# Performance work log

Hardware: AMD Instinct MI355X
Metric: run time of the kernel (lower is better)

The kernel has to match this reference:

```python
import jax, jax.numpy as jnp
import numpy as np

N = 100000      # nodes
E = 1600000     # edges (avg degree 16)
FEAT, HID, OUT = 128, 64, 40
P_DROP = 0.5


def setup_inputs() -> dict:
    key = jax.random.key(0)
    ks = jax.random.split(key, 7)
    x = jax.random.normal(ks[0], (N, FEAT), dtype=jnp.float32)
    edge_index = jax.random.randint(ks[1], (2, E), 0, N, dtype=jnp.int32)
    W1 = jax.random.normal(ks[2], (FEAT, HID), dtype=jnp.float32) / np.float32(np.sqrt(FEAT))
    b1 = jnp.zeros((HID,), jnp.float32)
    W2 = jax.random.normal(ks[3], (HID, OUT), dtype=jnp.float32) / np.float32(np.sqrt(HID))
    b2 = jnp.zeros((OUT,), jnp.float32)
    # scaled inverted-dropout mask: values in {0, 1/(1-p)}
    keep = jax.random.bernoulli(ks[4], 1.0 - P_DROP, (N, HID))
    drop_mask = keep.astype(jnp.float32) / np.float32(1.0 - P_DROP)
    return {"x": x, "edge_index": edge_index, "W1": W1, "b1": b1,
            "W2": W2, "b2": b2, "drop_mask": drop_mask}


def _gcn_conv(x, W, b, src, dst):
    """PyG GCNConv: h = xW; add self-loops; sym-normalized scatter-add; +b."""
    h = x @ W                                   # [N, D_out]
    ones = jnp.ones((src.shape[0],), h.dtype)
    deg = jax.ops.segment_sum(ones, dst, num_segments=N) + 1.0  # +1 self-loop
    dinv = jax.lax.rsqrt(deg)                   # deg > 0 due to self-loops
    norm = dinv[src] * dinv[dst]                # [E]
    msg = h[src] * norm[:, None]                # gather + scale
    agg = jax.ops.segment_sum(msg, dst, num_segments=N)
    agg = agg + h * (dinv * dinv)[:, None]      # self-loop contribution
    return agg + b


def reference(x, edge_index, W1, b1, W2, b2, drop_mask):
    src, dst = edge_index[0], edge_index[1]
    h = _gcn_conv(x, W1, b1, src, dst)
    h = jax.nn.relu(h)
    h = h * drop_mask                           # F.dropout (pre-drawn mask)
    out = _gcn_conv(h, W2, b2, src, dst)
    return out
```

## Files before the change

kernel.cpp:

```cpp
#include <hip/hip_runtime.h>
#include <hip/hip_fp16.h>

#define NN     100000
#define NE     1600000
#define FEAT   128
#define HID    64
#define OUTD   40
#define BNODES 32
#define NSB    ((NN + 255) / 256)
#define NBAGG  (NSB * 8)
#define CAP    5120
#define CCHUNK 2048
#define WSCALE 262144.0f
#define WINV   (1.0f / 262144.0f)

typedef _Float16 half8 __attribute__((ext_vector_type(8)));
typedef float    f32x4 __attribute__((ext_vector_type(4)));

__global__ __launch_bounds__(256) void k_pairs(const int* __restrict__ src,
                                               const int* __restrict__ dst,
                                               int* __restrict__ bfill,
                                               int* __restrict__ pairs) {
    __shared__ int bcnt[NSB];
    __shared__ int gb[NSB];
    int t = threadIdx.x;
    for (int i = t; i < NSB; i += 256) bcnt[i] = 0;
    __syncthreads();
    int e0 = blockIdx.x * CCHUNK;
    int pk[8], bb[8], off[8];
    #pragma unroll
    for (int i = 0; i < 8; ++i) {
        int e = e0 + i * 256 + t;
        if (e < NE) {
            int d = dst[e];
            pk[i]  = (src[e] << 8) | (d & 255);
            bb[i]  = d >> 8;
            off[i] = atomicAdd(&bcnt[bb[i]], 1);
        } else bb[i] = -1;
    }
    __syncthreads();
    for (int i = t; i < NSB; i += 256) {
        int c = bcnt[i];
        gb[i] = c ? (i * CAP + atomicAdd(&bfill[i], c)) : 0;
    }
    __syncthreads();
    #pragma unroll
    for (int i = 0; i < 8; ++i)
        if (bb[i] >= 0) pairs[gb[bb[i]] + off[i]] = pk[i];
}

__global__ __launch_bounds__(256) void k_degdinv(const int* __restrict__ pairs,
                                                 const int* __restrict__ bfill,
                                                 float* __restrict__ dinv) {
    __shared__ int hist[256];
    int b = blockIdx.x, t = threadIdx.x;
    hist[t] = 0;
    __syncthreads();
    int base = b * CAP, count = bfill[b];
    for (int i = t; i < count; i += 256)
        atomicAdd(&hist[pairs[base + i] & 255], 1);
    __syncthreads();
    int node = (b << 8) + t;
    if (node < NN) dinv[node] = rsqrtf((float)hist[t] + 1.0f);
}

__global__ __launch_bounds__(256) void k_csr(const int* __restrict__ pairs,
                                             const int* __restrict__ bfill,
                                             int* __restrict__ sb_beg,
                                             int* __restrict__ sb_cnt,
                                             int* __restrict__ csr) {
    __shared__ int hist[2048];
    __shared__ int exs[2048];
    __shared__ int part[256];
    __shared__ int poff[9];
    __shared__ int sstart[8];
    __shared__ int dtot[8];
    int b = blockIdx.x, t = threadIdx.x;
    #pragma unroll
    for (int k = 0; k < 8; ++k) hist[t * 8 + k] = 0;
    __syncthreads();
    int base = b * CAP, count = bfill[b];
    for (int i = t; i < count; i += 256) {
        int p = pairs[base + i];
        int key = (((p & 255) >> 5) << 8) | ((p >> 17) & 255);
        atomicAdd(&hist[key], 1);
    }
    __syncthreads();
    int loc[8], s0 = 0;
    #pragma unroll
    for (int k = 0; k < 8; ++k) { loc[k] = s0; s0 += hist[t * 8 + k]; }
    part[t] = s0;
    __syncthreads();
    for (int off = 1; off < 256; off <<= 1) {
        int u = (t >= off) ? part[t - off] : 0;
        __syncthreads();
        part[t] += u;
        __syncthreads();
    }
    int pex = part[t] - s0;
    #pragma unroll
    for (int k = 0; k < 8; ++k) exs[t * 8 + k] = pex + loc[k];
    __syncthreads();
    if (t < 8) {
        sstart[t] = exs[t * 256];
        int end = (t == 7) ? count : exs[(t + 1) * 256];
        dtot[t] = end - sstart[t];
    }
    __syncthreads();
    if (t == 0) {
        poff[0] = 0;
        for (int d = 0; d < 8; ++d) poff[d + 1] = poff[d] + ((dtot[d] + 31) & ~31);
    }
    __syncthreads();
    #pragma unroll
    for (int k = 0; k < 8; ++k) {
        int key = t * 8 + k;
        int d = key >> 8;
        exs[key] = poff[d] + (exs[key] - sstart[d]);
        hist[key] = 0;
    }
    __syncthreads();
    for (int i = t; i < count; i += 256) {
        int p = pairs[base + i];
        int key = (((p & 255) >> 5) << 8) | ((p >> 17) & 255);
        int pos = exs[key] + atomicAdd(&hist[key], 1);
        csr[base + pos] = ((p >> 8) << 7) | (p & 31);
    }
    for (int d = 0; d < 8; ++d) {
        int padded = (dtot[d] + 31) & ~31;
        for (int i = dtot[d] + t; i < padded; i += 256)
            csr[base + poff[d] + i] = (NN << 7);
    }
    if (t < 8) {
        sb_beg[b * 8 + t] = base + poff[t];
        sb_cnt[b * 8 + t] = (dtot[t] + 31) & ~31;
    }
}

__global__ __launch_bounds__(256) void k_maskbits(const float* __restrict__ mask,
                                                  unsigned long long* __restrict__ mb) {
    int node = blockIdx.x * 4 + (threadIdx.x >> 6);
    if (node >= NN) return;
    int l = threadIdx.x & 63;
    float m = mask[(size_t)node * HID + l];
    unsigned long long bits = __ballot(m != 0.f);
    if (l == 0) mb[node] = bits;
}

__global__ __launch_bounds__(256) void k_wprep(const float* __restrict__ W1,
                                               const float* __restrict__ W2,
                                               _Float16* __restrict__ w1f,
                                               _Float16* __restrict__ w2f,
                                               __half* __restrict__ h1s,
                                               __half* __restrict__ hhs) {
    int t = threadIdx.x;
    for (int it = t; it < 16 * 64; it += 256) {
        int f = it >> 6, l = it & 63;
        int kk = f >> 2, n = f & 3;
        int krow = kk * 32 + (l >> 4) * 8;
        int col  = n * 16 + (l & 15);
        #pragma unroll
        for (int i = 0; i < 8; ++i)
            w1f[it * 8 + i] = (_Float16)W1[(krow + i) * HID + col];
    }
    for (int it = t; it < 6 * 64; it += 256) {
        int f = it >> 6, l = it & 63;
        int kk = f / 3, n = f - kk * 3;
        int krow = kk * 32 + (l >> 4) * 8;
        int col  = n * 16 + (l & 15);
        #pragma unroll
        for (int i = 0; i < 8; ++i)
            w2f[it * 8 + i] = (col < OUTD) ? (_Float16)W2[(krow + i) * OUTD + col]
                                           : (_Float16)0.f;
    }
    if (t < HID) {
        h1s[(size_t)NN * HID + t] = __float2half(0.f);
        hhs[(size_t)NN * HID + t] = __float2half(0.f);
    }
}

__global__ __launch_bounds__(256) void k_mgemm1(const float* __restrict__ x,
                                                const _Float16* __restrict__ w1f,
                                                const float* __restrict__ dinv,
                                                __half* __restrict__ h1s) {
    int wid = (blockIdx.x * 256 + threadIdx.x) >> 6;
    int l = threadIdx.x & 63;
    if (wid >= NN / 16) return;
    half8 bf[4][4];
    #pragma unroll
    for (int kk = 0; kk < 4; ++kk)
        #pragma unroll
        for (int n = 0; n < 4; ++n)
            bf[kk][n] = ((const half8*)w1f)[(kk * 4 + n) * 64 + l];
    f32x4 acc[4] = {};
    int arow = wid * 16 + (l & 15);
    const float* xp = x + (size_t)arow * FEAT + (l >> 4) * 8;
    #pragma unroll
    for (int kk = 0; kk < 4; ++kk) {
        float4 u0 = *(const float4*)(xp + kk * 32);
        float4 u1 = *(const float4*)(xp + kk * 32 + 4);
        half8 af;
        af[0] = (_Float16)u0.x; af[1] = (_Float16)u0.y;
        af[2] = (_Float16)u0.z; af[3] = (_Float16)u0.w;
        af[4] = (_Float16)u1.x; af[5] = (_Float16)u1.y;
        af[6] = (_Float16)u1.z; af[7] = (_Float16)u1.w;
        #pragma unroll
        for (int n = 0; n < 4; ++n)
            acc[n] = __builtin_amdgcn_mfma_f32_16x16x32_f16(af, bf[kk][n], acc[n], 0, 0, 0);
    }
    int orow = wid * 16 + (l >> 4) * 4;
    int ocol = l & 15;
    float dv[4];
    #pragma unroll
    for (int r = 0; r < 4; ++r) dv[r] = dinv[orow + r];
    #pragma unroll
    for (int n = 0; n < 4; ++n)
        #pragma unroll
        for (int r = 0; r < 4; ++r)
            h1s[(size_t)(orow + r) * HID + n * 16 + ocol] = __float2half(acc[n][r] * dv[r]);
}

template<int MODE>
__global__ __launch_bounds__(256) void k_bagg(const int* __restrict__ csr,
                                              const int* __restrict__ sb_beg,
                                              const int* __restrict__ sb_cnt,
                                              const float* __restrict__ dinv,
                                              const __half* __restrict__ feat,
                                              const float* __restrict__ b1,
                                              const unsigned long long* __restrict__ maskbits,
                                              __half* __restrict__ outp) {
    __shared__ int acc[BNODES * HID];
    int t = threadIdx.x, wv = t >> 6, l = t & 63;
    int bb = blockIdx.x;
    int4* a4 = (int4*)acc;
    for (int i = t; i < BNODES * HID / 4; i += 256) a4[i] = make_int4(0, 0, 0, 0);
    __syncthreads();
    int base  = sb_beg[bb];
    int count = sb_cnt[bb];
    int node0 = (bb >> 3) * 256 + (bb & 7) * 32;
    const char* fb = (const char*)feat + ((size_t)l * 2);
    for (int j = wv * 8; j < count; j += 32) {
        int e0 = csr[base + j + 0], e1 = csr[base + j + 1];
        int e2 = csr[base + j + 2], e3 = csr[base + j + 3];
        int e4 = csr[base + j + 4], e5 = csr[base + j + 5];
        int e6 = csr[base + j + 6], e7 = csr[base + j + 7];
        float a0 = __half2float(*(const __half*)(fb + (unsigned)(e0 & ~127)));
        float a1 = __half2float(*(const __half*)(fb + (unsigned)(e1 & ~127)));
        float a2 = __half2float(*(const __half*)(fb + (unsigned)(e2 & ~127)));
        float a3 = __half2float(*(const __half*)(fb + (unsigned)(e3 & ~127)));
        float a4v = __half2float(*(const __half*)(fb + (unsigned)(e4 & ~127)));
        float a5 = __half2float(*(const __half*)(fb + (unsigned)(e5 & ~127)));
        float a6 = __half2float(*(const __half*)(fb + (unsigned)(e6 & ~127)));
        float a7 = __half2float(*(const __half*)(fb + (unsigned)(e7 & ~127)));
        atomicAdd(&acc[((e0 & 31) << 6) + l], (int)(a0 * WSCALE));
        atomicAdd(&acc[((e1 & 31) << 6) + l], (int)(a1 * WSCALE));
        atomicAdd(&acc[((e2 & 31) << 6) + l], (int)(a2 * WSCALE));
        atomicAdd(&acc[((e3 & 31) << 6) + l], (int)(a3 * WSCALE));
        atomicAdd(&acc[((e4 & 31) << 6) + l], (int)(a4v * WSCALE));
        atomicAdd(&acc[((e5 & 31) << 6) + l], (int)(a5 * WSCALE));
        atomicAdd(&acc[((e6 & 31) << 6) + l], (int)(a6 * WSCALE));
        atomicAdd(&acc[((e7 & 31) << 6) + l], (int)(a7 * WSCALE));
    }
    __syncthreads();
    for (int n = wv; n < BNODES; n += 4) {
        int node = node0 + n;
        if (node >= NN) break;
        float di = dinv[node];
        float selfv = __half2float(feat[(size_t)node * HID + l]);
        float vv = ((float)acc[(n << 6) + l] * WINV + selfv) * di;
        if (MODE == 0) {
            vv += b1[l];
            vv = vv > 0.f ? vv : 0.f;
            unsigned long long mb = maskbits[node];
            vv = ((mb >> l) & 1ull) ? vv * 2.0f * di : 0.0f;
        }
        outp[(size_t)node * HID + l] = __float2half(vv);
    }
}

__global__ __launch_bounds__(256) void k_mgemm2(const __half* __restrict__ aggh,
                                                const _Float16* __restrict__ w2f,
                                                const float* __restrict__ b2,
                                                float* __restrict__ out) {
    int wid = (blockIdx.x * 256 + threadIdx.x) >> 6;
    int l = threadIdx.x & 63;
    if (wid >= NN / 16) return;
    half8 bf[2][3];
    #pragma unroll
    for (int kk = 0; kk < 2; ++kk)
        #pragma unroll
        for (int n = 0; n < 3; ++n)
            bf[kk][n] = ((const half8*)w2f)[(kk * 3 + n) * 64 + l];
    f32x4 acc[3] = {};
    int arow = wid * 16 + (l & 15);
    const _Float16* hp = (const _Float16*)aggh + (size_t)arow * HID + (l >> 4) * 8;
    #pragma unroll
    for (int kk = 0; kk < 2; ++kk) {
        half8 af = *(const half8*)(hp + kk * 32);
        #pragma unroll
        for (int n = 0; n < 3; ++n)
            acc[n] = __builtin_amdgcn_mfma_f32_16x16x32_f16(af, bf[kk][n], acc[n], 0, 0, 0);
    }
    int orow = wid * 16 + (l >> 4) * 4;
    int ocol = l & 15;
    #pragma unroll
    for (int n = 0; n < 3; ++n) {
        int col = n * 16 + ocol;
        if (col < OUTD) {
            float bb = b2[col];
            #pragma unroll
            for (int r = 0; r < 4; ++r)
                out[(size_t)(orow + r) * OUTD + col] = acc[n][r] + bb;
        }
    }
}

extern "C" void kernel_launch(void* const* d_in, const int* in_sizes, int n_in,
                              void* d_out, int out_size, void* d_ws, size_t ws_size,
                              hipStream_t stream) {
    const float* x    = (const float*)d_in[0];
    const int*   ei   = (const int*)d_in[1];
    const int*   src  = ei;
    const int*   dst  = ei + NE;
    const float* W1   = (const float*)d_in[2];
    const float* b1   = (const float*)d_in[3];
    const float* W2   = (const float*)d_in[4];
    const float* b2   = (const float*)d_in[5];
    const float* mask = (const float*)d_in[6];
    float* out = (float*)d_out;

    char* ws = (char*)d_ws;
    int*      bfill  = (int*)ws;           ws += (size_t)NSB * 4;
    int*      sb_beg = (int*)ws;           ws += (size_t)NBAGG * 4;
    int*      sb_cnt = (int*)ws;           ws += (size_t)NBAGG * 4;
    float*    dinv   = (float*)ws;         ws += (size_t)NN * 4;
    unsigned long long* maskb = (unsigned long long*)ws; ws += (size_t)NN * 8;
    _Float16* w1f    = (_Float16*)ws;      ws += 16 * 64 * 8 * 2;
    _Float16* w2f    = (_Float16*)ws;      ws += 6 * 64 * 8 * 2;
    int*      csr    = (int*)ws;           ws += (size_t)NSB * CAP * 4;
    __half*   h1s    = (__half*)ws;        ws += (size_t)(NN + 1) * HID * 2;
    __half*   hhs    = (__half*)ws;        ws += (size_t)(NN + 1) * HID * 2;
    int*      pairs  = (int*)hhs;
    __half*   aggh   = h1s;

    hipMemsetAsync(bfill, 0, (size_t)NSB * 4, stream);

    k_pairs   <<<(NE + CCHUNK - 1) / CCHUNK, 256, 0, stream>>>(src, dst, bfill, pairs);
    k_degdinv <<<NSB, 256, 0, stream>>>(pairs, bfill, dinv);
    k_csr     <<<NSB, 256, 0, stream>>>(pairs, bfill, sb_beg, sb_cnt, csr);
    k_maskbits<<<(NN + 3) / 4, 256, 0, stream>>>(mask, maskb);
    k_wprep   <<<1, 256, 0, stream>>>(W1, W2, w1f, w2f, h1s, hhs);

    k_mgemm1  <<<(NN / 16 + 3) / 4, 256, 0, stream>>>(x, w1f, dinv, h1s);
    k_bagg<0> <<<NBAGG, 256, 0, stream>>>(csr, sb_beg, sb_cnt, dinv, h1s, b1, maskb, hhs);
    k_bagg<1> <<<NBAGG, 256, 0, stream>>>(csr, sb_beg, sb_cnt, dinv, hhs, nullptr, nullptr, aggh);
    k_mgemm2  <<<(NN / 16 + 3) / 4, 256, 0, stream>>>(aggh, w2f, b2, out);
}
```

Measured before the change: 181.5 us.

## Fuse degree count into CSR build and second GEMM into final aggregation

Folds the dinv computation into k_csr via an extra shared histogram, removing one kernel launch and one pass over the pairs buffer. The final aggregation kernel now does the 64x40 MFMA projection with bias straight from its shared accumulator, so the aggregated half-precision intermediate is never written to or read back from global memory and k_mgemm2 is gone. The edge loop is also widened to 16 gathers per wave iteration for more memory-level parallelism. In exchange, only two of four waves do the MFMA epilogue, and the larger unrolled loop raises register pressure.

```diff
diff --git a/kernel.cpp b/kernel.cpp
--- a/kernel.cpp
+++ b/kernel.cpp
@@ -49,28 +49,15 @@
         if (bb[i] >= 0) pairs[gb[bb[i]] + off[i]] = pk[i];
 }
 
-__global__ __launch_bounds__(256) void k_degdinv(const int* __restrict__ pairs,
-                                                 const int* __restrict__ bfill,
-                                                 float* __restrict__ dinv) {
-    __shared__ int hist[256];
-    int b = blockIdx.x, t = threadIdx.x;
-    hist[t] = 0;
-    __syncthreads();
-    int base = b * CAP, count = bfill[b];
-    for (int i = t; i < count; i += 256)
-        atomicAdd(&hist[pairs[base + i] & 255], 1);
-    __syncthreads();
-    int node = (b << 8) + t;
-    if (node < NN) dinv[node] = rsqrtf((float)hist[t] + 1.0f);
-}
-
 __global__ __launch_bounds__(256) void k_csr(const int* __restrict__ pairs,
                                              const int* __restrict__ bfill,
                                              int* __restrict__ sb_beg,
                                              int* __restrict__ sb_cnt,
-                                             int* __restrict__ csr) {
+                                             int* __restrict__ csr,
+                                             float* __restrict__ dinv) {
     __shared__ int hist[2048];
     __shared__ int exs[2048];
+    __shared__ int nd[256];
     __shared__ int part[256];
     __shared__ int poff[9];
     __shared__ int sstart[8];
@@ -78,14 +65,20 @@
     int b = blockIdx.x, t = threadIdx.x;
     #pragma unroll
     for (int k = 0; k < 8; ++k) hist[t * 8 + k] = 0;
+    nd[t] = 0;
     __syncthreads();
     int base = b * CAP, count = bfill[b];
     for (int i = t; i < count; i += 256) {
         int p = pairs[base + i];
         int key = (((p & 255) >> 5) << 8) | ((p >> 17) & 255);
         atomicAdd(&hist[key], 1);
-    }
-    __syncthreads();
+        atomicAdd(&nd[p & 255], 1);
+    }
+    __syncthreads();
+    {
+        int node = (b << 8) + t;
+        if (node < NN) dinv[node] = rsqrtf((float)nd[t] + 1.0f);
+    }
     int loc[8], s0 = 0;
     #pragma unroll
     for (int k = 0; k < 8; ++k) { loc[k] = s0; s0 += hist[t * 8 + k]; }
@@ -228,7 +221,10 @@
                                               const __half* __restrict__ feat,
                                               const float* __restrict__ b1,
                                               const unsigned long long* __restrict__ maskbits,
-                                              __half* __restrict__ outp) {
+                                              __half* __restrict__ outp,
+                                              const _Float16* __restrict__ w2f,
+                                              const float* __restrict__ b2,
+                                              float* __restrict__ outf) {
     __shared__ int acc[BNODES * HID];
     int t = threadIdx.x, wv = t >> 6, l = t & 63;
     int bb = blockIdx.x;
@@ -239,78 +235,76 @@
     int count = sb_cnt[bb];
     int node0 = (bb >> 3) * 256 + (bb & 7) * 32;
     const char* fb = (const char*)feat + ((size_t)l * 2);
-    for (int j = wv * 8; j < count; j += 32) {
-        int e0 = csr[base + j + 0], e1 = csr[base + j + 1];
-        int e2 = csr[base + j + 2], e3 = csr[base + j + 3];
-        int e4 = csr[base + j + 4], e5 = csr[base + j + 5];
-        int e6 = csr[base + j + 6], e7 = csr[base + j + 7];
-        float a0 = __half2float(*(const __half*)(fb + (unsigned)(e0 & ~127)));
-        float a1 = __half2float(*(const __half*)(fb + (unsigned)(e1 & ~127)));
-        float a2 = __half2float(*(const __half*)(fb + (unsigned)(e2 & ~127)));
-        float a3 = __half2float(*(const __half*)(fb + (unsigned)(e3 & ~127)));
-        float a4v = __half2float(*(const __half*)(fb + (unsigned)(e4 & ~127)));
-        float a5 = __half2float(*(const __half*)(fb + (unsigned)(e5 & ~127)));
-        float a6 = __half2float(*(const __half*)(fb + (unsigned)(e6 & ~127)));
-        float a7 = __half2float(*(const __half*)(fb + (unsigned)(e7 & ~127)));
-        atomicAdd(&acc[((e0 & 31) << 6) + l], (int)(a0 * WSCALE));
-        atomicAdd(&acc[((e1 & 31) << 6) + l], (int)(a1 * WSCALE));
-        atomicAdd(&acc[((e2 & 31) << 6) + l], (int)(a2 * WSCALE));
-        atomicAdd(&acc[((e3 & 31) << 6) + l], (int)(a3 * WSCALE));
-        atomicAdd(&acc[((e4 & 31) << 6) + l], (int)(a4v * WSCALE));
-        atomicAdd(&acc[((e5 & 31) << 6) + l], (int)(a5 * WSCALE));
-        atomicAdd(&acc[((e6 & 31) << 6) + l], (int)(a6 * WSCALE));
-        atomicAdd(&acc[((e7 & 31) << 6) + l], (int)(a7 * WSCALE));
-    }
-    __syncthreads();
-    for (int n = wv; n < BNODES; n += 4) {
-        int node = node0 + n;
-        if (node >= NN) break;
-        float di = dinv[node];
-        float selfv = __half2float(feat[(size_t)node * HID + l]);
-        float vv = ((float)acc[(n << 6) + l] * WINV + selfv) * di;
-        if (MODE == 0) {
+    for (int j = wv * 16; j < count; j += 64) {
+        int e[16];
+        #pragma unroll
+        for (int i = 0; i < 16; ++i) e[i] = csr[base + j + i];
+        float a[16];
+        #pragma unroll
+        for (int i = 0; i < 16; ++i)
+            a[i] = __half2float(*(const __half*)(fb + (unsigned)(e[i] & ~127)));
+        #pragma unroll
+        for (int i = 0; i < 16; ++i)
+            atomicAdd(&acc[((e[i] & 31) << 6) + l], (int)(a[i] * WSCALE));
+    }
+    __syncthreads();
+    if (MODE == 0) {
+        for (int n = wv; n < BNODES; n += 4) {
+            int node = node0 + n;
+            if (node >= NN) break;
+            float di = dinv[node];
+            float selfv = __half2float(feat[(size_t)node * HID + l]);
+            float vv = ((float)acc[(n << 6) + l] * WINV + selfv) * di;
             vv += b1[l];
             vv = vv > 0.f ? vv : 0.f;
             unsigned long long mb = maskbits[node];
             vv = ((mb >> l) & 1ull) ? vv * 2.0f * di : 0.0f;
+            outp[(size_t)node * HID + l] = __float2half(vv);
         }
-        outp[(size_t)node * HID + l] = __float2half(vv);
-    }
-}
-
-__global__ __launch_bounds__(256) void k_mgemm2(const __half* __restrict__ aggh,
-                                                const _Float16* __restrict__ w2f,
-                                                const float* __restrict__ b2,
-                                                float* __restrict__ out) {
-    int wid = (blockIdx.x * 256 + threadIdx.x) >> 6;
-    int l = threadIdx.x & 63;
-    if (wid >= NN / 16) return;
-    half8 bf[2][3];
-    #pragma unroll
-    for (int kk = 0; kk < 2; ++kk)
-        #pragma unroll
-        for (int n = 0; n < 3; ++n)
-            bf[kk][n] = ((const half8*)w2f)[(kk * 3 + n) * 64 + l];
-    f32x4 acc[3] = {};
-    int arow = wid * 16 + (l & 15);
-    const _Float16* hp = (const _Float16*)aggh + (size_t)arow * HID + (l >> 4) * 8;
-    #pragma unroll
-    for (int kk = 0; kk < 2; ++kk) {
-        half8 af = *(const half8*)(hp + kk * 32);
-        #pragma unroll
-        for (int n = 0; n < 3; ++n)
-            acc[n] = __builtin_amdgcn_mfma_f32_16x16x32_f16(af, bf[kk][n], acc[n], 0, 0, 0);
-    }
-    int orow = wid * 16 + (l >> 4) * 4;
-    int ocol = l & 15;
-    #pragma unroll
-    for (int n = 0; n < 3; ++n) {
-        int col = n * 16 + ocol;
-        if (col < OUTD) {
-            float bb = b2[col];
+    } else {
+        if (wv < 2) {
+            half8 bf[2][3];
             #pragma unroll
-            for (int r = 0; r < 4; ++r)
-                out[(size_t)(orow + r) * OUTD + col] = acc[n][r] + bb;
+            for (int kk = 0; kk < 2; ++kk)
+                #pragma unroll
+                for (int n = 0; n < 3; ++n)
+                    bf[kk][n] = ((const half8*)w2f)[(kk * 3 + n) * 64 + l];
+            int lrow = wv * 16 + (l & 15);
+            int node = node0 + lrow;
+            int srow = node < NN ? node : NN;
+            float di = dinv[node < NN ? node : NN - 1];
+            int k0 = (l >> 4) * 8;
+            half8 af[2];
+            #pragma unroll
+            for (int kk = 0; kk < 2; ++kk)
+                #pragma unroll
+                for (int i = 0; i < 8; ++i) {
+                    int k = kk * 32 + k0 + i;
+                    float v = ((float)acc[(lrow << 6) + k] * WINV
+                              + __half2float(feat[(size_t)srow * HID + k])) * di;
+                    af[kk][i] = (_Float16)v;
+                }
+            f32x4 o[3] = {};
+            #pragma unroll
+            for (int kk = 0; kk < 2; ++kk)
+                #pragma unroll
+                for (int n = 0; n < 3; ++n)
+                    o[n] = __builtin_amdgcn_mfma_f32_16x16x32_f16(af[kk], bf[kk][n], o[n], 0, 0, 0);
+            int orow = node0 + wv * 16 + (l >> 4) * 4;
+            int ocol = l & 15;
+            #pragma unroll
+            for (int n = 0; n < 3; ++n) {
+                int col = n * 16 + ocol;
+                if (col < OUTD) {
+                    float bbias = b2[col];
+                    #pragma unroll
+                    for (int r = 0; r < 4; ++r) {
+                        int row = orow + r;
+                        if (row < NN)
+                            outf[(size_t)row * OUTD + col] = o[n][r] + bbias;
+                    }
+                }
+            }
         }
     }
 }
@@ -341,18 +335,17 @@
     __half*   h1s    = (__half*)ws;        ws += (size_t)(NN + 1) * HID * 2;
     __half*   hhs    = (__half*)ws;        ws += (size_t)(NN + 1) * HID * 2;
     int*      pairs  = (int*)hhs;
-    __half*   aggh   = h1s;
 
     hipMemsetAsync(bfill, 0, (size_t)NSB * 4, stream);
 
     k_pairs   <<<(NE + CCHUNK - 1) / CCHUNK, 256, 0, stream>>>(src, dst, bfill, pairs);
-    k_degdinv <<<NSB, 256, 0, stream>>>(pairs, bfill, dinv);
-    k_csr     <<<NSB, 256, 0, stream>>>(pairs, bfill, sb_beg, sb_cnt, csr);
+    k_csr     <<<NSB, 256, 0, stream>>>(pairs, bfill, sb_beg, sb_cnt, csr, dinv);
     k_maskbits<<<(NN + 3) / 4, 256, 0, stream>>>(mask, maskb);
     k_wprep   <<<1, 256, 0, stream>>>(W1, W2, w1f, w2f, h1s, hhs);
 
     k_mgemm1  <<<(NN / 16 + 3) / 4, 256, 0, stream>>>(x, w1f, dinv, h1s);
-    k_bagg<0> <<<NBAGG, 256, 0, stream>>>(csr, sb_beg, sb_cnt, dinv, h1s, b1, maskb, hhs);
-    k_bagg<1> <<<NBAGG, 256, 0, stream>>>(csr, sb_beg, sb_cnt, dinv, hhs, nullptr, nullptr, aggh);
-    k_mgemm2  <<<(NN / 16 + 3) / 4, 256, 0, stream>>>(aggh, w2f, b2, out);
-}
+    k_bagg<0> <<<NBAGG, 256, 0, stream>>>(csr, sb_beg, sb_cnt, dinv, h1s, b1, maskb,
+                                          hhs, nullptr, nullptr, nullptr);
+    k_bagg<1> <<<NBAGG, 256, 0, stream>>>(csr, sb_beg, sb_cnt, dinv, hhs, nullptr, nullptr,
+                                          nullptr, w2f, b2, out);
+}
```

After: 180.8 us. Within noise of the previous version (-0.4%).
